# Optimization experiments

Hardware: AMD Instinct MI355X
Metric: run time of the kernel (lower is better)

The kernel has to match this reference:

```python
import jax, jax.numpy as jnp
import numpy as np

MEMORY_SIZE = 32768
DIM_K = 256
DIM_V = 256
B = 2048
OLD_SIZE = 16384


def setup_inputs() -> dict:
    key = jax.random.key(0)
    k1, k2, k3, k4, k5 = jax.random.split(key, 5)
    return {
        "q": jax.random.normal(k1, (B, DIM_K), dtype=jnp.float32),
        "k": jax.random.normal(k2, (B, DIM_K), dtype=jnp.float32),
        "v": jax.random.normal(k3, (B, DIM_V), dtype=jnp.float32),
        "K_cache": jax.random.normal(k4, (MEMORY_SIZE, DIM_K), dtype=jnp.float32),
        "V_cache": jax.random.normal(k5, (MEMORY_SIZE, DIM_V), dtype=jnp.float32),
        "old_size": OLD_SIZE,
    }


def reference(q, k, v, K_cache, V_cache, old_size):
    b, dim_k = q.shape
    new_size = old_size + b  # static python int
    # write the new chunk of keys/values into the cache
    K = jax.lax.dynamic_update_slice(K_cache, k, (old_size, 0))
    V = jax.lax.dynamic_update_slice(V_cache, v, (old_size, 0))
    Kv = K[:new_size]  # [new_size, dim_k]
    Vv = V[:new_size]  # [new_size, dim_v]
    # scaled dot-product scores: [b, new_size]
    scores = (q @ Kv.T) * (1.0 / (dim_k ** 0.5))
    # causal mask: query i (global pos old_size+i) may attend keys j <= old_size+i
    key_idx = jnp.arange(new_size)[None, :]
    query_idx = jnp.arange(old_size, new_size)[:, None]
    scores = jnp.where(key_idx > query_idx, -jnp.inf, scores)
    p = jax.nn.softmax(scores, axis=-1)
    return p @ Vv  # [b, dim_v]
```

## Files before the change

### kernel.cpp

```cpp
#include <hip/hip_runtime.h>
#include <hip/hip_bf16.h>
#include <cstdint>

typedef __attribute__((ext_vector_type(8))) short s8b;
typedef __attribute__((ext_vector_type(4))) short s4b;
typedef __attribute__((ext_vector_type(2))) short s2b;
typedef __attribute__((ext_vector_type(4))) float f4v;

#define MFMA16(a,b,c) __builtin_amdgcn_mfma_f32_16x16x32_bf16((a),(b),(c),0,0,0)

#define OLDN   16384
#define NEWB   2048
#define DHEAD  256
#define NTOTAL 18432
#define SCALE  0.0625f

#define KSTR  264
#define VSTR  40
#define PSTR  40

static __device__ __forceinline__ short f2bf(float f) {
    unsigned u = __float_as_uint(f);
    unsigned r = (u + 0x7fffu + ((u >> 16) & 1u)) >> 16;
    return (short)r;
}

__global__ void cvt_kernel(const float* __restrict__ Kc, const float* __restrict__ kn,
                           const float* __restrict__ Vc, const float* __restrict__ vn,
                           s8b* __restrict__ Kb, s8b* __restrict__ Vb) {
    int idx8 = blockIdx.x * 256 + threadIdx.x;
    int idx  = idx8 * 8;
    int row  = idx >> 8;
    int col  = idx & 255;
    const float* src;
    if (blockIdx.y == 0)
        src = (row < OLDN) ? (Kc + (size_t)row * DHEAD + col)
                           : (kn + (size_t)(row - OLDN) * DHEAD + col);
    else
        src = (row < OLDN) ? (Vc + (size_t)row * DHEAD + col)
                           : (vn + (size_t)(row - OLDN) * DHEAD + col);
    float4 f0 = *(const float4*)src;
    float4 f1 = *(const float4*)(src + 4);
    s8b o;
    o[0]=f2bf(f0.x); o[1]=f2bf(f0.y); o[2]=f2bf(f0.z); o[3]=f2bf(f0.w);
    o[4]=f2bf(f1.x); o[5]=f2bf(f1.y); o[6]=f2bf(f1.z); o[7]=f2bf(f1.w);
    (blockIdx.y == 0 ? Kb : Vb)[idx8] = o;
}

__global__ __launch_bounds__(256, 3)
void attn_kernel(const float* __restrict__ q,
                 const short* __restrict__ Kb, const short* __restrict__ Vb,
                 float* __restrict__ OP, float* __restrict__ L, int SPLIT) {
    __shared__ short K_lds[32 * KSTR];
    __shared__ short Vt_lds[DHEAD * VSTR];
    __shared__ short P_lds[4][16 * PSTR];

    const int bx   = blockIdx.x;
    const int s    = bx % SPLIT;
    const int qb   = bx / SPLIT;
    const int q0   = qb * 64;
    const int tid  = threadIdx.x;
    const int w    = tid >> 6;
    const int lane = tid & 63;
    const int ln   = lane & 15;
    const int quad = lane >> 4;

    s8b qf[8];
    {
        const int qrow = q0 + w * 16 + ln;
        const float* qp = q + (size_t)qrow * DHEAD + quad * 8;
#pragma unroll
        for (int kt = 0; kt < 8; ++kt) {
            float4 f0 = *(const float4*)(qp + kt * 32);
            float4 f1 = *(const float4*)(qp + kt * 32 + 4);
            s8b o;
            o[0]=f2bf(f0.x); o[1]=f2bf(f0.y); o[2]=f2bf(f0.z); o[3]=f2bf(f0.w);
            o[4]=f2bf(f1.x); o[5]=f2bf(f1.y); o[6]=f2bf(f1.z); o[7]=f2bf(f1.w);
            qf[kt] = o;
        }
    }

    f4v Oa[16];
#pragma unroll
    for (int i = 0; i < 16; ++i) Oa[i] = (f4v){0.f, 0.f, 0.f, 0.f};
    float l_r[4] = {0.f, 0.f, 0.f, 0.f};

    const int krow = tid >> 3;
    const int kkey = (krow < 16) ? 2 * krow : 2 * krow - 31;
    const int kcb  = (tid & 7) * 8;
    const int va   = tid & 3;
    const int vd   = (tid >> 2) * 4;

    const int nt_total = (OLDN + q0 + 64) >> 5;
    const int tb  = nt_total / SPLIT;
    const int rem = nt_total % SPLIT;
    const int t0  = s * tb + (s < rem ? s : rem);
    const int tcnt = tb + (s < rem ? 1 : 0);

    const int kmax0 = OLDN + q0 + w * 16 + quad * 4;
    const int kwave = OLDN + q0 + w * 16;

    for (int t = t0; t < t0 + tcnt; ++t) {
        const int kk = t << 5;
        __syncthreads();
        {
            const s8b* src = (const s8b*)(Kb + (size_t)(kk + kkey) * DHEAD + kcb);
            short* dst = &K_lds[krow * KSTR + kcb];
#pragma unroll
            for (int i = 0; i < 4; ++i)
                *(s8b*)(dst + i * 64) = src[i * 8];
        }
        {
            const short* vp = Vb + (size_t)(kk + va * 8) * DHEAD + vd;
            s4b ld[8];
#pragma unroll
            for (int j = 0; j < 8; ++j)
                ld[j] = *(const s4b*)(vp + (size_t)j * DHEAD);
#pragma unroll
            for (int r = 0; r < 4; ++r) {
                s8b o;
#pragma unroll
                for (int j = 0; j < 8; ++j) o[j] = ld[j][r];
                *(s8b*)&Vt_lds[(vd + r) * VSTR + va * 8] = o;
            }
        }
        __syncthreads();

        f4v sa = (f4v){0.f,0.f,0.f,0.f};
        f4v sb = (f4v){0.f,0.f,0.f,0.f};
#pragma unroll
        for (int kt = 0; kt < 8; ++kt) {
            s8b k0 = *(const s8b*)&K_lds[ ln       * KSTR + kt * 32 + quad * 8];
            s8b k1 = *(const s8b*)&K_lds[(ln + 16) * KSTR + kt * 32 + quad * 8];
            sa = MFMA16(qf[kt], k0, sa);
            sb = MFMA16(qf[kt], k1, sb);
        }

        const bool domask = (kk + 31 > kwave);
#pragma unroll
        for (int reg = 0; reg < 4; ++reg) {
            float e0 = __expf(sa[reg] * SCALE);
            float e1 = __expf(sb[reg] * SCALE);
            if (domask) {
                if (kk + 2 * ln     > kmax0 + reg) e0 = 0.f;
                if (kk + 2 * ln + 1 > kmax0 + reg) e1 = 0.f;
            }
            l_r[reg] += e0 + e1;
            s2b p; p[0] = f2bf(e0); p[1] = f2bf(e1);
            *(s2b*)&P_lds[w][(quad * 4 + reg) * PSTR + 2 * ln] = p;
        }

        asm volatile("s_waitcnt lgkmcnt(0)" ::: "memory");
        s8b pf = *(const s8b*)&P_lds[w][ln * PSTR + quad * 8];

#pragma unroll
        for (int nt = 0; nt < 16; ++nt) {
            s8b vf = *(const s8b*)&Vt_lds[(nt * 16 + ln) * VSTR + quad * 8];
            Oa[nt] = MFMA16(pf, vf, Oa[nt]);
        }
    }

#pragma unroll
    for (int reg = 0; reg < 4; ++reg) {
#pragma unroll
        for (int off = 1; off < 16; off <<= 1)
            l_r[reg] += __shfl_xor(l_r[reg], off);
    }

    const int orow = q0 + w * 16;
    const size_t sbase = (size_t)s * NEWB;
#pragma unroll
    for (int nt = 0; nt < 16; ++nt)
#pragma unroll
        for (int reg = 0; reg < 4; ++reg)
            OP[(sbase + orow + quad * 4 + reg) * DHEAD + nt * 16 + ln] = Oa[nt][reg];
    if (ln == 0) {
#pragma unroll
        for (int reg = 0; reg < 4; ++reg)
            L[sbase + orow + quad * 4 + reg] = l_r[reg];
    }
}

__global__ void combine_kernel(const float* __restrict__ OP, const float* __restrict__ L,
                               float* __restrict__ out, int SPLIT) {
    const int row = blockIdx.x;
    const int col = threadIdx.x;
    float num = 0.f, den = 0.f;
    for (int s = 0; s < SPLIT; ++s) {
        size_t r = (size_t)s * NEWB + row;
        num += OP[r * DHEAD + col];
        den += L[r];
    }
    out[(size_t)row * DHEAD + col] = num / den;
}

extern "C" void kernel_launch(void* const* d_in, const int* in_sizes, int n_in,
                              void* d_out, int out_size, void* d_ws, size_t ws_size,
                              hipStream_t stream) {
    const float* q  = (const float*)d_in[0];
    const float* kn = (const float*)d_in[1];
    const float* vn = (const float*)d_in[2];
    const float* Kc = (const float*)d_in[3];
    const float* Vc = (const float*)d_in[4];
    float* out = (float*)d_out;

    char* ws = (char*)d_ws;
    const size_t KB_BYTES = (size_t)NTOTAL * DHEAD * 2;
    short* Kb = (short*)(ws);
    short* Vb = (short*)(ws + KB_BYTES);
    const size_t PART_BASE = 2 * KB_BYTES;

    const size_t per_split = (size_t)NEWB * DHEAD * 4 + (size_t)NEWB * 4;
    size_t avail = (ws_size > PART_BASE) ? (ws_size - PART_BASE) : 0;
    int SPLIT = (int)(avail / per_split);
    if (SPLIT > 24) SPLIT = 24;
    if (SPLIT < 1)  SPLIT = 1;

    float* OP = (float*)(ws + PART_BASE);
    float* L  = (float*)(ws + PART_BASE + (size_t)SPLIT * NEWB * DHEAD * 4);

    cvt_kernel<<<dim3(NTOTAL * DHEAD / (256 * 8), 2), 256, 0, stream>>>(Kc, kn, Vc, vn,
                                                                        (s8b*)Kb, (s8b*)Vb);
    attn_kernel<<<32 * SPLIT, 256, 0, stream>>>(q, Kb, Vb, OP, L, SPLIT);
    combine_kernel<<<NEWB, 256, 0, stream>>>(OP, L, out, SPLIT);
}
```

Measured before the change: 195.4 us.

## Switch attention to 32x32 MFMA tiles with 128-query blocks and register-resident P

Replaces the 16x16x32 MFMA tiling with 32x32x16 MFMA, so each wave handles 32 query rows and a block covers 128 queries. This halves how often each K/V tile is loaded per query. The score accumulator layout is computed transposed (K as A operand), which lets the exponentiated probabilities feed the PV MFMA straight from registers and removes the P round-trip through LDS. It also uses exp2 with a prescaled constant, raises the split cap to 32, and lowers launch bounds to 2 blocks/SM to fit the larger accumulators, which may reduce occupancy.

```diff
diff --git a/kernel.cpp b/kernel.cpp
--- a/kernel.cpp
+++ b/kernel.cpp
@@ -2,22 +2,20 @@
 #include <hip/hip_bf16.h>
 #include <cstdint>
 
-typedef __attribute__((ext_vector_type(8))) short s8b;
-typedef __attribute__((ext_vector_type(4))) short s4b;
-typedef __attribute__((ext_vector_type(2))) short s2b;
-typedef __attribute__((ext_vector_type(4))) float f4v;
-
-#define MFMA16(a,b,c) __builtin_amdgcn_mfma_f32_16x16x32_bf16((a),(b),(c),0,0,0)
+typedef __attribute__((ext_vector_type(8)))  short s8b;
+typedef __attribute__((ext_vector_type(4)))  short s4b;
+typedef __attribute__((ext_vector_type(16))) float f16v;
+
+#define MFMA32(a,b,c) __builtin_amdgcn_mfma_f32_32x32x16_bf16((a),(b),(c),0,0,0)
 
 #define OLDN   16384
 #define NEWB   2048
 #define DHEAD  256
 #define NTOTAL 18432
-#define SCALE  0.0625f
+#define EXPSC  0.09016844005556021f
 
 #define KSTR  264
 #define VSTR  40
-#define PSTR  40
 
 static __device__ __forceinline__ short f2bf(float f) {
     unsigned u = __float_as_uint(f);
@@ -47,138 +45,133 @@
     (blockIdx.y == 0 ? Kb : Vb)[idx8] = o;
 }
 
-__global__ __launch_bounds__(256, 3)
+__global__ __launch_bounds__(256, 2)
 void attn_kernel(const float* __restrict__ q,
                  const short* __restrict__ Kb, const short* __restrict__ Vb,
                  float* __restrict__ OP, float* __restrict__ L, int SPLIT) {
     __shared__ short K_lds[32 * KSTR];
     __shared__ short Vt_lds[DHEAD * VSTR];
-    __shared__ short P_lds[4][16 * PSTR];
 
     const int bx   = blockIdx.x;
     const int s    = bx % SPLIT;
     const int qb   = bx / SPLIT;
-    const int q0   = qb * 64;
+    const int q0   = qb * 128;
     const int tid  = threadIdx.x;
     const int w    = tid >> 6;
     const int lane = tid & 63;
-    const int ln   = lane & 15;
-    const int quad = lane >> 4;
-
-    s8b qf[8];
+    const int lc   = lane & 31;
+    const int h    = lane >> 5;
+
+    s8b qf[16];
     {
-        const int qrow = q0 + w * 16 + ln;
-        const float* qp = q + (size_t)qrow * DHEAD + quad * 8;
-#pragma unroll
-        for (int kt = 0; kt < 8; ++kt) {
-            float4 f0 = *(const float4*)(qp + kt * 32);
-            float4 f1 = *(const float4*)(qp + kt * 32 + 4);
+        const int qrow = q0 + 32 * w + lc;
+        const float* qp = q + (size_t)qrow * DHEAD + 8 * h;
+#pragma unroll
+        for (int c = 0; c < 16; ++c) {
+            float4 f0 = *(const float4*)(qp + 16 * c);
+            float4 f1 = *(const float4*)(qp + 16 * c + 4);
             s8b o;
             o[0]=f2bf(f0.x); o[1]=f2bf(f0.y); o[2]=f2bf(f0.z); o[3]=f2bf(f0.w);
             o[4]=f2bf(f1.x); o[5]=f2bf(f1.y); o[6]=f2bf(f1.z); o[7]=f2bf(f1.w);
-            qf[kt] = o;
+            qf[c] = o;
         }
     }
 
-    f4v Oa[16];
-#pragma unroll
-    for (int i = 0; i < 16; ++i) Oa[i] = (f4v){0.f, 0.f, 0.f, 0.f};
-    float l_r[4] = {0.f, 0.f, 0.f, 0.f};
+    f16v acc[8];
+#pragma unroll
+    for (int c = 0; c < 8; ++c)
+#pragma unroll
+        for (int r = 0; r < 16; ++r) acc[c][r] = 0.f;
+    float lsum = 0.f;
 
     const int krow = tid >> 3;
-    const int kkey = (krow < 16) ? 2 * krow : 2 * krow - 31;
     const int kcb  = (tid & 7) * 8;
     const int va   = tid & 3;
     const int vd   = (tid >> 2) * 4;
-
-    const int nt_total = (OLDN + q0 + 64) >> 5;
+    const int vkb  = 16 * (va >> 1) + 4 * (va & 1);
+
+    const int nt_total = (OLDN + q0 + 128) >> 5;
     const int tb  = nt_total / SPLIT;
     const int rem = nt_total % SPLIT;
     const int t0  = s * tb + (s < rem ? s : rem);
     const int tcnt = tb + (s < rem ? 1 : 0);
 
-    const int kmax0 = OLDN + q0 + w * 16 + quad * 4;
-    const int kwave = OLDN + q0 + w * 16;
+    const int qbase = OLDN + q0 + 32 * w;
 
     for (int t = t0; t < t0 + tcnt; ++t) {
         const int kk = t << 5;
         __syncthreads();
         {
-            const s8b* src = (const s8b*)(Kb + (size_t)(kk + kkey) * DHEAD + kcb);
+            const s8b* src = (const s8b*)(Kb + (size_t)(kk + krow) * DHEAD + kcb);
             short* dst = &K_lds[krow * KSTR + kcb];
 #pragma unroll
             for (int i = 0; i < 4; ++i)
                 *(s8b*)(dst + i * 64) = src[i * 8];
         }
         {
-            const short* vp = Vb + (size_t)(kk + va * 8) * DHEAD + vd;
             s4b ld[8];
 #pragma unroll
             for (int j = 0; j < 8; ++j)
-                ld[j] = *(const s4b*)(vp + (size_t)j * DHEAD);
+                ld[j] = *(const s4b*)(Vb + (size_t)(kk + vkb + (j & 3) + 8 * (j >> 2)) * DHEAD + vd);
 #pragma unroll
             for (int r = 0; r < 4; ++r) {
                 s8b o;
 #pragma unroll
                 for (int j = 0; j < 8; ++j) o[j] = ld[j][r];
-                *(s8b*)&Vt_lds[(vd + r) * VSTR + va * 8] = o;
+                *(s8b*)&Vt_lds[(vd + r) * VSTR + 8 * va] = o;
             }
         }
         __syncthreads();
 
-        f4v sa = (f4v){0.f,0.f,0.f,0.f};
-        f4v sb = (f4v){0.f,0.f,0.f,0.f};
-#pragma unroll
-        for (int kt = 0; kt < 8; ++kt) {
-            s8b k0 = *(const s8b*)&K_lds[ ln       * KSTR + kt * 32 + quad * 8];
-            s8b k1 = *(const s8b*)&K_lds[(ln + 16) * KSTR + kt * 32 + quad * 8];
-            sa = MFMA16(qf[kt], k0, sa);
-            sb = MFMA16(qf[kt], k1, sb);
-        }
-
-        const bool domask = (kk + 31 > kwave);
-#pragma unroll
-        for (int reg = 0; reg < 4; ++reg) {
-            float e0 = __expf(sa[reg] * SCALE);
-            float e1 = __expf(sb[reg] * SCALE);
+        f16v sacc;
+#pragma unroll
+        for (int r = 0; r < 16; ++r) sacc[r] = 0.f;
+#pragma unroll
+        for (int c = 0; c < 16; ++c) {
+            s8b kf = *(const s8b*)&K_lds[lc * KSTR + 16 * c + 8 * h];
+            sacc = MFMA32(kf, qf[c], sacc);
+        }
+
+        const bool domask = (kk + 31 > qbase);
+        float e[16];
+#pragma unroll
+        for (int r = 0; r < 16; ++r) {
+            float ev = __builtin_exp2f(sacc[r] * EXPSC);
             if (domask) {
-                if (kk + 2 * ln     > kmax0 + reg) e0 = 0.f;
-                if (kk + 2 * ln + 1 > kmax0 + reg) e1 = 0.f;
+                int key = kk + (r & 3) + 8 * (r >> 2) + 4 * h;
+                if (key > qbase + lc) ev = 0.f;
             }
-            l_r[reg] += e0 + e1;
-            s2b p; p[0] = f2bf(e0); p[1] = f2bf(e1);
-            *(s2b*)&P_lds[w][(quad * 4 + reg) * PSTR + 2 * ln] = p;
-        }
-
-        asm volatile("s_waitcnt lgkmcnt(0)" ::: "memory");
-        s8b pf = *(const s8b*)&P_lds[w][ln * PSTR + quad * 8];
-
-#pragma unroll
-        for (int nt = 0; nt < 16; ++nt) {
-            s8b vf = *(const s8b*)&Vt_lds[(nt * 16 + ln) * VSTR + quad * 8];
-            Oa[nt] = MFMA16(pf, vf, Oa[nt]);
+            e[r] = ev;
+            lsum += ev;
+        }
+        s8b pf0, pf1;
+#pragma unroll
+        for (int j = 0; j < 8; ++j) { pf0[j] = f2bf(e[j]); pf1[j] = f2bf(e[8 + j]); }
+
+#pragma unroll
+        for (int c = 0; c < 8; ++c) {
+            const short* vrow = &Vt_lds[(32 * c + lc) * VSTR];
+            s8b v0 = *(const s8b*)(vrow + 8 * h);
+            s8b v1 = *(const s8b*)(vrow + 16 + 8 * h);
+            acc[c] = MFMA32(v0, pf0, acc[c]);
+            acc[c] = MFMA32(v1, pf1, acc[c]);
         }
     }
 
-#pragma unroll
-    for (int reg = 0; reg < 4; ++reg) {
-#pragma unroll
-        for (int off = 1; off < 16; off <<= 1)
-            l_r[reg] += __shfl_xor(l_r[reg], off);
-    }
-
-    const int orow = q0 + w * 16;
+    lsum += __shfl_xor(lsum, 32);
+
+    const int qrow = q0 + 32 * w + lc;
     const size_t sbase = (size_t)s * NEWB;
-#pragma unroll
-    for (int nt = 0; nt < 16; ++nt)
-#pragma unroll
-        for (int reg = 0; reg < 4; ++reg)
-            OP[(sbase + orow + quad * 4 + reg) * DHEAD + nt * 16 + ln] = Oa[nt][reg];
-    if (ln == 0) {
-#pragma unroll
-        for (int reg = 0; reg < 4; ++reg)
-            L[sbase + orow + quad * 4 + reg] = l_r[reg];
-    }
+    float* op_row = OP + (sbase + qrow) * DHEAD;
+#pragma unroll
+    for (int c = 0; c < 8; ++c)
+#pragma unroll
+        for (int g = 0; g < 4; ++g) {
+            float4 o = {acc[c][4 * g], acc[c][4 * g + 1], acc[c][4 * g + 2], acc[c][4 * g + 3]};
+            *(float4*)(op_row + 32 * c + 8 * g + 4 * h) = o;
+        }
+    if (h == 0)
+        L[sbase + qrow] = lsum;
 }
 
 __global__ void combine_kernel(const float* __restrict__ OP, const float* __restrict__ L,
@@ -213,7 +206,7 @@
     const size_t per_split = (size_t)NEWB * DHEAD * 4 + (size_t)NEWB * 4;
     size_t avail = (ws_size > PART_BASE) ? (ws_size - PART_BASE) : 0;
     int SPLIT = (int)(avail / per_split);
-    if (SPLIT > 24) SPLIT = 24;
+    if (SPLIT > 32) SPLIT = 32;
     if (SPLIT < 1)  SPLIT = 1;
 
     float* OP = (float*)(ws + PART_BASE);
@@ -221,6 +214,6 @@
 
     cvt_kernel<<<dim3(NTOTAL * DHEAD / (256 * 8), 2), 256, 0, stream>>>(Kc, kn, Vc, vn,
                                                                         (s8b*)Kb, (s8b*)Vb);
-    attn_kernel<<<32 * SPLIT, 256, 0, stream>>>(q, Kb, Vb, OP, L, SPLIT);
+    attn_kernel<<<16 * SPLIT, 256, 0, stream>>>(q, Kb, Vb, OP, L, SPLIT);
     combine_kernel<<<NEWB, 256, 0, stream>>>(OP, L, out, SPLIT);
 }
```

Measured after the change: 200.9 us. +2.8%, slower.
